# Kernel optimization log

Measured on AMD Instinct MI355X. Metric: run time of the kernel, lower is better.

## Reference

```python
import jax, jax.numpy as jnp
import numpy as np

N = 100000
E = 1600000
D_IN = 128
HID = 128
OUT = 64


def _sage_conv(x, edge_index, W_l, W_r, b, num_nodes):
    # PyG SAGEConv (aggr='mean'): out = lin_l(mean_{j in N(i)} x_j) + lin_r(x_i)
    src, dst = edge_index[0], edge_index[1]
    msgs = x[src]  # [E, d] gather from source nodes
    summed = jax.ops.segment_sum(msgs, dst, num_segments=num_nodes)  # [N, d]
    cnt = jax.ops.segment_sum(jnp.ones((msgs.shape[0],), x.dtype), dst, num_segments=num_nodes)
    agg = summed / jnp.maximum(cnt, 1.0)[:, None]  # mean; isolated nodes -> 0
    return agg @ W_l + b + x @ W_r


def setup_inputs() -> dict:
    key = jax.random.key(0)
    ks = jax.random.split(key, 8)
    x = jax.random.normal(ks[0], (N, D_IN), dtype=jnp.float32)
    edge_index = jax.random.randint(ks[1], (2, E), 0, N, dtype=jnp.int64)
    s1 = 1.0 / np.sqrt(D_IN)
    s2 = 1.0 / np.sqrt(HID)
    W_l1 = jax.random.uniform(ks[2], (D_IN, HID), jnp.float32, -s1, s1)
    W_r1 = jax.random.uniform(ks[3], (D_IN, HID), jnp.float32, -s1, s1)
    b1 = jnp.zeros((HID,), jnp.float32)
    W_l2 = jax.random.uniform(ks[4], (HID, OUT), jnp.float32, -s2, s2)
    W_r2 = jax.random.uniform(ks[5], (HID, OUT), jnp.float32, -s2, s2)
    b2 = jnp.zeros((OUT,), jnp.float32)
    return {"x": x, "edge_index": edge_index, "W_l1": W_l1, "W_r1": W_r1,
            "b1": b1, "W_l2": W_l2, "W_r2": W_r2, "b2": b2}


def reference(x, edge_index, W_l1, W_r1, b1, W_l2, W_r2, b2):
    h = _sage_conv(x, edge_index, W_l1, W_r1, b1, N)
    h = jax.nn.relu(h)
    out = _sage_conv(h, edge_index, W_l2, W_r2, b2, N)
    return out
```

## Files before the change

kernel.cpp:

```cpp
#include <hip/hip_runtime.h>
#include <hip/hip_fp16.h>

typedef __attribute__((ext_vector_type(8))) short bf16x8;
typedef __attribute__((ext_vector_type(4))) float f32x4;

__device__ __forceinline__ f32x4 mfma16(bf16x8 a, bf16x8 b, f32x4 c) {
    return __builtin_amdgcn_mfma_f32_16x16x32_bf16(a, b, c, 0, 0, 0);
}

__device__ __forceinline__ unsigned short bf16_rte(float f) {
    unsigned int u = __float_as_uint(f);
    unsigned int r = (u + 0x7FFFu + ((u >> 16) & 1u)) >> 16;
    return (unsigned short)r;
}
__device__ __forceinline__ float bf16_f(unsigned short h) {
    return __uint_as_float(((unsigned int)h) << 16);
}

__device__ __forceinline__ void split8h(bf16x8 raw, bf16x8& hi, bf16x8& lo) {
#pragma unroll
    for (int j = 0; j < 8; ++j) {
        float f = __half2float(__ushort_as_half((unsigned short)raw[j]));
        unsigned short h = bf16_rte(f);
        hi[j] = (short)h;
        lo[j] = (short)bf16_rte(f - bf16_f(h));
    }
}

__global__ void k_wconv(const float* __restrict__ W, unsigned short* __restrict__ hi,
                        unsigned short* __restrict__ lo, int K, int F) {
    int e = blockIdx.x * 256 + threadIdx.x;
    if (e >= K * F) return;
    int col = e / K, k = e - col * K;
    float v = W[(size_t)k * F + col];
    unsigned short h = bf16_rte(v);
    hi[e] = h;
    lo[e] = bf16_rte(v - bf16_f(h));
}

__global__ __launch_bounds__(256) void k_xconv(const float* __restrict__ x,
                                               unsigned short* __restrict__ x16,
                                               int total8) {
    int i = blockIdx.x * 256 + threadIdx.x;
    if (i >= total8) return;
    const float4* xp = (const float4*)x + (size_t)i * 2;
    float4 a = xp[0], b = xp[1];
    bf16x8 o;
    o[0] = (short)__half_as_ushort(__float2half_rn(a.x));
    o[1] = (short)__half_as_ushort(__float2half_rn(a.y));
    o[2] = (short)__half_as_ushort(__float2half_rn(a.z));
    o[3] = (short)__half_as_ushort(__float2half_rn(a.w));
    o[4] = (short)__half_as_ushort(__float2half_rn(b.x));
    o[5] = (short)__half_as_ushort(__float2half_rn(b.y));
    o[6] = (short)__half_as_ushort(__float2half_rn(b.z));
    o[7] = (short)__half_as_ushort(__float2half_rn(b.w));
    *(bf16x8*)&x16[(size_t)i * 8] = o;
}


#define MAXNB 1024

__global__ __launch_bounds__(256) void k_bcount(
    const int* __restrict__ dst, int* __restrict__ bcnt, int E, int chunk, int nb) {
    __shared__ int h[MAXNB];
    int t = threadIdx.x;
    for (int i = t; i < nb; i += 256) h[i] = 0;
    __syncthreads();
    int base = blockIdx.x * chunk;
    int end = min(base + chunk, E);
    for (int i = base + t; i < end; i += 256) atomicAdd(&h[dst[i] >> 7], 1);
    __syncthreads();
    for (int i = t; i < nb; i += 256)
        if (h[i]) atomicAdd(&bcnt[i], h[i]);
}

__global__ void k_bscan(const int* __restrict__ bcnt, int* __restrict__ boff,
                        int* __restrict__ bcur, int nb) {
    __shared__ int sh[1024];
    int t = threadIdx.x;
    int v = (t < nb) ? bcnt[t] : 0;
    sh[t] = v;
    __syncthreads();
    for (int off = 1; off < 1024; off <<= 1) {
        int u = (t >= off) ? sh[t - off] : 0;
        __syncthreads();
        sh[t] += u;
        __syncthreads();
    }
    if (t < nb) {
        int ex = sh[t] - v;
        boff[t] = ex;
        bcur[t] = ex;
    }
}

__global__ __launch_bounds__(256) void k_bscatter(
    const int* __restrict__ src, const int* __restrict__ dst,
    int* __restrict__ bcur, int2* __restrict__ pairs, int E, int chunk, int nb) {
    __shared__ int h[MAXNB];
    __shared__ int curs[MAXNB];
    int t = threadIdx.x;
    for (int i = t; i < nb; i += 256) h[i] = 0;
    __syncthreads();
    int base = blockIdx.x * chunk;
    int end = min(base + chunk, E);
    for (int i = base + t; i < end; i += 256) atomicAdd(&h[dst[i] >> 7], 1);
    __syncthreads();
    for (int i = t; i < nb; i += 256)
        curs[i] = h[i] ? atomicAdd(&bcur[i], h[i]) : 0;
    __syncthreads();
    for (int i = base + t; i < end; i += 256) {
        int d = dst[i];
        int p = atomicAdd(&curs[d >> 7], 1);
        pairs[p] = make_int2(d, src[i]);
    }
}

__global__ __launch_bounds__(256) void k_build(
    const int2* __restrict__ pairs, const int* __restrict__ boff,
    int* __restrict__ csr, int* __restrict__ start, int* __restrict__ deg,
    int n, int nb, int E) {
    __shared__ int scnt[128];
    __shared__ int soff[128];
    __shared__ int cur[128];
    int b = blockIdx.x;
    int t = threadIdx.x;
    int base = boff[b];
    int end = (b + 1 < nb) ? boff[b + 1] : E;
    if (t < 128) scnt[t] = 0;
    __syncthreads();
    for (int i = base + t; i < end; i += 256) {
        int2 e = pairs[i];
        atomicAdd(&scnt[e.x & 127], 1);
    }
    __syncthreads();
    if (t < 128) soff[t] = scnt[t];
    __syncthreads();
    for (int off = 1; off < 128; off <<= 1) {
        int val = 0;
        if (t < 128 && t >= off) val = soff[t - off];
        __syncthreads();
        if (t < 128) soff[t] += val;
        __syncthreads();
    }
    if (t < 128) {
        int c = scnt[t];
        int ex = soff[t] - c;
        int node = b * 128 + t;
        if (node < n) {
            start[node] = base + ex;
            deg[node] = c;
        }
        cur[t] = base + ex;
    }
    __syncthreads();
    for (int i = base + t; i < end; i += 256) {
        int2 e = pairs[i];
        int p = atomicAdd(&cur[e.x & 127], 1);
        csr[p] = e.y;
    }
}


#define SR 40

template <int FOUT, bool S0F32, bool OUT_H16>
__device__ __forceinline__ void gemm_dual_body(
    const float* __restrict__ X0f, const unsigned short* __restrict__ X0h,
    const unsigned short* __restrict__ X1h,
    const unsigned short* __restrict__ W0H, const unsigned short* __restrict__ W0L,
    const unsigned short* __restrict__ W1H, const unsigned short* __restrict__ W1L,
    const float* __restrict__ bias, unsigned short* __restrict__ dstH,
    float* __restrict__ dstF, int n) {
    constexpr int CT = FOUT / 64;
    __shared__ unsigned short aHi[4][64 * SR], aLo[4][64 * SR];

    int t = threadIdx.x;
    int wv = t >> 6, l = t & 63, q = l >> 4, nl = l & 15;
    int wc = wv * (FOUT / 4);
    int node0 = blockIdx.x * 64;
    int sn = t >> 2, q4 = t & 3;
    int gn = min(node0 + sn, n - 1);

    bf16x8 s1r[4];
    {
        const unsigned short* p = X1h + (size_t)gn * 128 + q4 * 8;
#pragma unroll
        for (int c = 0; c < 4; ++c) s1r[c] = *(const bf16x8*)(p + c * 32);
    }
    bf16x8 w1h0[CT], w1l0[CT];
#pragma unroll
    for (int uu = 0; uu < CT; ++uu) {
        int base = (wc + uu * 16 + nl) * 128 + q * 8;
        w1h0[uu] = *(const bf16x8*)&W1H[base];
        w1l0[uu] = *(const bf16x8*)&W1L[base];
    }

    if (S0F32) {
        const float4* ap = (const float4*)(X0f + (size_t)gn * 128);
        float4 xa[8];
#pragma unroll
        for (int c = 0; c < 4; ++c) {
            xa[c * 2]     = ap[c * 8 + q4 * 2];
            xa[c * 2 + 1] = ap[c * 8 + q4 * 2 + 1];
        }
        int base = sn * SR + q4 * 8;
#pragma unroll
        for (int c = 0; c < 4; ++c) {
            ushort4 hi, lo;
            float4 v = xa[c * 2];
            hi.x = bf16_rte(v.x); lo.x = bf16_rte(v.x - bf16_f(hi.x));
            hi.y = bf16_rte(v.y); lo.y = bf16_rte(v.y - bf16_f(hi.y));
            hi.z = bf16_rte(v.z); lo.z = bf16_rte(v.z - bf16_f(hi.z));
            hi.w = bf16_rte(v.w); lo.w = bf16_rte(v.w - bf16_f(hi.w));
            *(ushort4*)&aHi[c][base] = hi;
            *(ushort4*)&aLo[c][base] = lo;
            v = xa[c * 2 + 1];
            hi.x = bf16_rte(v.x); lo.x = bf16_rte(v.x - bf16_f(hi.x));
            hi.y = bf16_rte(v.y); lo.y = bf16_rte(v.y - bf16_f(hi.y));
            hi.z = bf16_rte(v.z); lo.z = bf16_rte(v.z - bf16_f(hi.z));
            hi.w = bf16_rte(v.w); lo.w = bf16_rte(v.w - bf16_f(hi.w));
            *(ushort4*)&aHi[c][base + 4] = hi;
            *(ushort4*)&aLo[c][base + 4] = lo;
        }
    } else {
        const unsigned short* p = X0h + (size_t)gn * 128 + q4 * 8;
        bf16x8 r[4];
#pragma unroll
        for (int c = 0; c < 4; ++c) r[c] = *(const bf16x8*)(p + c * 32);
        int base = sn * SR + q4 * 8;
#pragma unroll
        for (int c = 0; c < 4; ++c) {
            bf16x8 hi, lo;
            split8h(r[c], hi, lo);
            *(bf16x8*)&aHi[c][base] = hi;
            *(bf16x8*)&aLo[c][base] = lo;
        }
    }

    f32x4 acc[4][CT];
#pragma unroll
    for (int a = 0; a < 4; ++a)
#pragma unroll
        for (int b = 0; b < CT; ++b) acc[a][b] = (f32x4){0.f, 0.f, 0.f, 0.f};

    bf16x8 wh[2][CT], wl[2][CT];
#pragma unroll
    for (int uu = 0; uu < CT; ++uu) {
        int base = (wc + uu * 16 + nl) * 128 + q * 8;
        wh[0][uu] = *(const bf16x8*)&W0H[base];
        wl[0][uu] = *(const bf16x8*)&W0L[base];
    }
    __syncthreads();

#pragma unroll
    for (int c = 0; c < 4; ++c) {
        if (c < 3) {
#pragma unroll
            for (int uu = 0; uu < CT; ++uu) {
                int base = (wc + uu * 16 + nl) * 128 + (c + 1) * 32 + q * 8;
                wh[(c + 1) & 1][uu] = *(const bf16x8*)&W0H[base];
                wl[(c + 1) & 1][uu] = *(const bf16x8*)&W0L[base];
            }
        }
        bf16x8 ah[4], al[4];
#pragma unroll
        for (int tt = 0; tt < 4; ++tt) {
            int off = (tt * 16 + nl) * SR + q * 8;
            ah[tt] = *(const bf16x8*)&aHi[c][off];
            al[tt] = *(const bf16x8*)&aLo[c][off];
        }
        int cb = c & 1;
#pragma unroll
        for (int tt = 0; tt < 4; ++tt)
#pragma unroll
            for (int uu = 0; uu < CT; ++uu) {
                f32x4 a = acc[tt][uu];
                a = mfma16(al[tt], wh[cb][uu], a);
                a = mfma16(ah[tt], wl[cb][uu], a);
                a = mfma16(ah[tt], wh[cb][uu], a);
                acc[tt][uu] = a;
            }
    }
    __syncthreads();

    {
        int base = sn * SR + q4 * 8;
#pragma unroll
        for (int c = 0; c < 4; ++c) {
            bf16x8 hi, lo;
            split8h(s1r[c], hi, lo);
            *(bf16x8*)&aHi[c][base] = hi;
            *(bf16x8*)&aLo[c][base] = lo;
        }
    }
#pragma unroll
    for (int uu = 0; uu < CT; ++uu) { wh[0][uu] = w1h0[uu]; wl[0][uu] = w1l0[uu]; }
    __syncthreads();

#pragma unroll
    for (int c = 0; c < 4; ++c) {
        if (c < 3) {
#pragma unroll
            for (int uu = 0; uu < CT; ++uu) {
                int base = (wc + uu * 16 + nl) * 128 + (c + 1) * 32 + q * 8;
                wh[(c + 1) & 1][uu] = *(const bf16x8*)&W1H[base];
                wl[(c + 1) & 1][uu] = *(const bf16x8*)&W1L[base];
            }
        }
        bf16x8 ah[4], al[4];
#pragma unroll
        for (int tt = 0; tt < 4; ++tt) {
            int off = (tt * 16 + nl) * SR + q * 8;
            ah[tt] = *(const bf16x8*)&aHi[c][off];
            al[tt] = *(const bf16x8*)&aLo[c][off];
        }
        int cb = c & 1;
#pragma unroll
        for (int tt = 0; tt < 4; ++tt)
#pragma unroll
            for (int uu = 0; uu < CT; ++uu) {
                f32x4 a = acc[tt][uu];
                a = mfma16(al[tt], wh[cb][uu], a);
                a = mfma16(ah[tt], wl[cb][uu], a);
                a = mfma16(ah[tt], wh[cb][uu], a);
                acc[tt][uu] = a;
            }
    }
    __syncthreads();

    if (OUT_H16) {
        unsigned short* tb = &aHi[0][0];
#pragma unroll
        for (int uu = 0; uu < CT; ++uu) {
            int col = wc + uu * 16 + nl;
            float bv = bias[col];
#pragma unroll
            for (int tt = 0; tt < 4; ++tt)
#pragma unroll
                for (int r = 0; r < 4; ++r) {
                    float vv = fmaxf(acc[tt][uu][r] + bv, 0.f);
                    tb[(tt * 16 + q * 4 + r) * 136 + col] =
                        __half_as_ushort(__float2half_rn(vv));
                }
        }
        __syncthreads();
        int node = node0 + sn;
        if (node < n) {
            const unsigned short* sp = tb + sn * 136 + q4 * 32;
            unsigned short* dp = dstH + (size_t)node * 128 + q4 * 32;
#pragma unroll
            for (int i = 0; i < 4; ++i) *(bf16x8*)(dp + i * 8) = *(const bf16x8*)(sp + i * 8);
        }
    } else {
        float* tb = (float*)&aHi[0][0];
#pragma unroll
        for (int uu = 0; uu < CT; ++uu) {
            int col = wc + uu * 16 + nl;
            float bv = bias[col];
#pragma unroll
            for (int tt = 0; tt < 4; ++tt)
#pragma unroll
                for (int r = 0; r < 4; ++r)
                    tb[(tt * 16 + q * 4 + r) * 68 + col] = acc[tt][uu][r] + bv;
        }
        __syncthreads();
        int node = node0 + sn;
        if (node < n) {
            const float* sp = tb + sn * 68 + q4 * 16;
            float* dp = dstF + (size_t)node * 64 + q4 * 16;
#pragma unroll
            for (int i = 0; i < 4; ++i) *(float4*)(dp + i * 4) = *(const float4*)(sp + i * 4);
        }
    }
}

__global__ __launch_bounds__(256, 2) void gemm1f(
    const float* __restrict__ X, const unsigned short* __restrict__ XM,
    const unsigned short* WrH, const unsigned short* WrL,
    const unsigned short* WlH, const unsigned short* WlL,
    const float* __restrict__ bias, unsigned short* __restrict__ h16, int n) {
    gemm_dual_body<128, true, true>(X, nullptr, XM, WrH, WrL, WlH, WlL, bias, h16, nullptr, n);
}

__global__ __launch_bounds__(256, 2) void gemm2f(
    const unsigned short* __restrict__ H, const unsigned short* __restrict__ HM,
    const unsigned short* WrH, const unsigned short* WrL,
    const unsigned short* WlH, const unsigned short* WlL,
    const float* __restrict__ bias, float* __restrict__ out, int n) {
    gemm_dual_body<64, false, false>(nullptr, H, HM, WrH, WrL, WlH, WlL, bias, nullptr, out, n);
}

__global__ void aggF(const unsigned short* __restrict__ tab, const int* __restrict__ csr,
                     const int* __restrict__ start, const int* __restrict__ deg,
                     unsigned short* __restrict__ outm, int n) {
    int gid = blockIdx.x * blockDim.x + threadIdx.x;
    int wave = gid >> 6, lane = gid & 63;
    int half = lane >> 5, fl = lane & 31;
    int node = wave * 2 + half;
    if (node >= n) return;
    int s = start[node], d = deg[node];
    const float2* u2 = (const float2*)tab;
    float4 A = {0.f, 0.f, 0.f, 0.f}, B = {0.f, 0.f, 0.f, 0.f};
    int j = 0;
    for (; j + 4 <= d; j += 4) {
        int i0 = csr[s + j], i1 = csr[s + j + 1], i2 = csr[s + j + 2], i3 = csr[s + j + 3];
        float2 r0 = u2[(size_t)i0 * 32 + fl];
        float2 r1 = u2[(size_t)i1 * 32 + fl];
        float2 r2 = u2[(size_t)i2 * 32 + fl];
        float2 r3 = u2[(size_t)i3 * 32 + fl];
        float2 a0 = __half22float2(*(const __half2*)&r0.x), b0 = __half22float2(*(const __half2*)&r0.y);
        float2 a1 = __half22float2(*(const __half2*)&r1.x), b1 = __half22float2(*(const __half2*)&r1.y);
        float2 a2 = __half22float2(*(const __half2*)&r2.x), b2 = __half22float2(*(const __half2*)&r2.y);
        float2 a3 = __half22float2(*(const __half2*)&r3.x), b3 = __half22float2(*(const __half2*)&r3.y);
        A.x += a0.x + a1.x; A.y += a0.y + a1.y;
        A.z += b0.x + b1.x; A.w += b0.y + b1.y;
        B.x += a2.x + a3.x; B.y += a2.y + a3.y;
        B.z += b2.x + b3.x; B.w += b2.y + b3.y;
    }
    for (; j < d; ++j) {
        float2 r0 = u2[(size_t)csr[s + j] * 32 + fl];
        float2 a0 = __half22float2(*(const __half2*)&r0.x), b0 = __half22float2(*(const __half2*)&r0.y);
        A.x += a0.x; A.y += a0.y; A.z += b0.x; A.w += b0.y;
    }
    float inv = 1.0f / (float)max(d, 1);
    float mx = (A.x + B.x) * inv, my = (A.y + B.y) * inv;
    float mz = (A.z + B.z) * inv, mw = (A.w + B.w) * inv;
    __half2 h01 = __floats2half2_rn(mx, my);
    __half2 h23 = __floats2half2_rn(mz, mw);
    uint2 w;
    w.x = *(unsigned int*)&h01;
    w.y = *(unsigned int*)&h23;
    *(uint2*)&outm[(size_t)node * 128 + fl * 4] = w;
}


extern "C" void kernel_launch(void* const* d_in, const int* in_sizes, int n_in,
                              void* d_out, int out_size, void* d_ws, size_t ws_size,
                              hipStream_t stream) {
    const float* x   = (const float*)d_in[0];
    const int*   ei  = (const int*)d_in[1];
    const float* Wl1 = (const float*)d_in[2];
    const float* Wr1 = (const float*)d_in[3];
    const float* b1  = (const float*)d_in[4];
    const float* Wl2 = (const float*)d_in[5];
    const float* Wr2 = (const float*)d_in[6];
    const float* b2  = (const float*)d_in[7];
    float* out = (float*)d_out;

    int Nn = in_sizes[0] / 128;
    int E  = in_sizes[1] / 2;
    const int* src = ei;
    const int* dst = ei + E;
    int nb = (Nn + 127) / 128;

    char* ws = (char*)d_ws;
    auto alloc = [&](size_t bytes) -> char* {
        char* pp = ws;
        ws += (bytes + 255) / 256 * 256;
        return pp;
    };
    int* bcnt   = (int*)alloc((size_t)nb * 4);
    int* boff   = (int*)alloc((size_t)nb * 4);
    int* bcur   = (int*)alloc((size_t)nb * 4);
    int* start  = (int*)alloc((size_t)Nn * 4);
    int* deg    = (int*)alloc((size_t)Nn * 4);
    int* csr    = (int*)alloc((size_t)E * 4);
    unsigned short* x16  = (unsigned short*)alloc((size_t)Nn * 128 * 2);
    unsigned short* xm16 = (unsigned short*)alloc((size_t)Nn * 128 * 2);
    unsigned short* h16  = (unsigned short*)alloc((size_t)Nn * 128 * 2);
    unsigned short* hm16 = (unsigned short*)alloc((size_t)Nn * 128 * 2);
    unsigned short* w1ah = (unsigned short*)alloc(128 * 128 * 2);
    unsigned short* w1al = (unsigned short*)alloc(128 * 128 * 2);
    unsigned short* w1bh = (unsigned short*)alloc(128 * 128 * 2);
    unsigned short* w1bl = (unsigned short*)alloc(128 * 128 * 2);
    unsigned short* w2ah = (unsigned short*)alloc(64 * 128 * 2);
    unsigned short* w2al = (unsigned short*)alloc(64 * 128 * 2);
    unsigned short* w2bh = (unsigned short*)alloc(64 * 128 * 2);
    unsigned short* w2bl = (unsigned short*)alloc(64 * 128 * 2);
    int2* pairs = (int2*)hm16;

    hipMemsetAsync(bcnt, 0, (size_t)nb * 4, stream);

    k_wconv<<<64, 256, 0, stream>>>(Wl1, w1ah, w1al, 128, 128);
    k_wconv<<<64, 256, 0, stream>>>(Wr1, w1bh, w1bl, 128, 128);
    k_wconv<<<32, 256, 0, stream>>>(Wl2, w2ah, w2al, 128, 64);
    k_wconv<<<32, 256, 0, stream>>>(Wr2, w2bh, w2bl, 128, 64);
    k_xconv<<<(Nn * 16 + 255) / 256, 256, 0, stream>>>(x, x16, Nn * 16);

    int chunk = (E + 255) / 256;
    k_bcount<<<256, 256, 0, stream>>>(dst, bcnt, E, chunk, nb);
    k_bscan<<<1, 1024, 0, stream>>>(bcnt, boff, bcur, nb);
    k_bscatter<<<256, 256, 0, stream>>>(src, dst, bcur, pairs, E, chunk, nb);
    k_build<<<nb, 256, 0, stream>>>(pairs, boff, csr, start, deg, Nn, nb, E);

    int gb = (Nn + 63) / 64;
    aggF<<<(Nn + 7) / 8, 256, 0, stream>>>(x16, csr, start, deg, xm16, Nn);
    gemm1f<<<gb, 256, 0, stream>>>(x, xm16, w1bh, w1bl, w1ah, w1al, b1, h16, Nn);
    aggF<<<(Nn + 7) / 8, 256, 0, stream>>>(h16, csr, start, deg, hm16, Nn);
    gemm2f<<<gb, 256, 0, stream>>>(h16, hm16, w2bh, w2bl, w2ah, w2al, b2, out, Nn);
}
```

Baseline: 377.4 us.

## Merge weight conversions into one launch, feed fp16 x to gemm1, prefetch CSR indices

Four weight-conversion launches are merged into a single kernel that dispatches on block index. gemm1 now reads the fp16 copy of x instead of the fp32 input, which halves that read and reuses the split path already used by gemm2. The cost is an fp16 rounding of x before the self term, which may affect accuracy. The aggregation loop also software-prefetches the next four neighbour indices so index loads overlap the feature gathers.

```diff
diff --git a/kernel.cpp b/kernel.cpp
--- a/kernel.cpp
+++ b/kernel.cpp
@@ -27,11 +27,23 @@
     }
 }
 
-__global__ void k_wconv(const float* __restrict__ W, unsigned short* __restrict__ hi,
-                        unsigned short* __restrict__ lo, int K, int F) {
-    int e = blockIdx.x * 256 + threadIdx.x;
-    if (e >= K * F) return;
-    int col = e / K, k = e - col * K;
+__global__ __launch_bounds__(256) void k_wconv_all(
+    const float* __restrict__ Wl1, const float* __restrict__ Wr1,
+    const float* __restrict__ Wl2, const float* __restrict__ Wr2,
+    unsigned short* __restrict__ w1ah, unsigned short* __restrict__ w1al,
+    unsigned short* __restrict__ w1bh, unsigned short* __restrict__ w1bl,
+    unsigned short* __restrict__ w2ah, unsigned short* __restrict__ w2al,
+    unsigned short* __restrict__ w2bh, unsigned short* __restrict__ w2bl) {
+    int b = blockIdx.x;
+    const float* W;
+    unsigned short *hi, *lo;
+    int F, e;
+    if (b < 64)       { W = Wl1; hi = w1ah; lo = w1al; F = 128; e = b * 256 + threadIdx.x; }
+    else if (b < 128) { W = Wr1; hi = w1bh; lo = w1bl; F = 128; e = (b - 64) * 256 + threadIdx.x; }
+    else if (b < 160) { W = Wl2; hi = w2ah; lo = w2al; F = 64;  e = (b - 128) * 256 + threadIdx.x; }
+    else              { W = Wr2; hi = w2bh; lo = w2bl; F = 64;  e = (b - 160) * 256 + threadIdx.x; }
+    if (e >= 128 * F) return;
+    int col = e >> 7, k = e & 127;
     float v = W[(size_t)k * F + col];
     unsigned short h = bf16_rte(v);
     hi[e] = h;
@@ -164,10 +176,9 @@
 
 #define SR 40
 
-template <int FOUT, bool S0F32, bool OUT_H16>
+template <int FOUT, bool OUT_H16>
 __device__ __forceinline__ void gemm_dual_body(
-    const float* __restrict__ X0f, const unsigned short* __restrict__ X0h,
-    const unsigned short* __restrict__ X1h,
+    const unsigned short* __restrict__ X0h, const unsigned short* __restrict__ X1h,
     const unsigned short* __restrict__ W0H, const unsigned short* __restrict__ W0L,
     const unsigned short* __restrict__ W1H, const unsigned short* __restrict__ W1L,
     const float* __restrict__ bias, unsigned short* __restrict__ dstH,
@@ -196,34 +207,7 @@
         w1l0[uu] = *(const bf16x8*)&W1L[base];
     }
 
-    if (S0F32) {
-        const float4* ap = (const float4*)(X0f + (size_t)gn * 128);
-        float4 xa[8];
-#pragma unroll
-        for (int c = 0; c < 4; ++c) {
-            xa[c * 2]     = ap[c * 8 + q4 * 2];
-            xa[c * 2 + 1] = ap[c * 8 + q4 * 2 + 1];
-        }
-        int base = sn * SR + q4 * 8;
-#pragma unroll
-        for (int c = 0; c < 4; ++c) {
-            ushort4 hi, lo;
-            float4 v = xa[c * 2];
-            hi.x = bf16_rte(v.x); lo.x = bf16_rte(v.x - bf16_f(hi.x));
-            hi.y = bf16_rte(v.y); lo.y = bf16_rte(v.y - bf16_f(hi.y));
-            hi.z = bf16_rte(v.z); lo.z = bf16_rte(v.z - bf16_f(hi.z));
-            hi.w = bf16_rte(v.w); lo.w = bf16_rte(v.w - bf16_f(hi.w));
-            *(ushort4*)&aHi[c][base] = hi;
-            *(ushort4*)&aLo[c][base] = lo;
-            v = xa[c * 2 + 1];
-            hi.x = bf16_rte(v.x); lo.x = bf16_rte(v.x - bf16_f(hi.x));
-            hi.y = bf16_rte(v.y); lo.y = bf16_rte(v.y - bf16_f(hi.y));
-            hi.z = bf16_rte(v.z); lo.z = bf16_rte(v.z - bf16_f(hi.z));
-            hi.w = bf16_rte(v.w); lo.w = bf16_rte(v.w - bf16_f(hi.w));
-            *(ushort4*)&aHi[c][base + 4] = hi;
-            *(ushort4*)&aLo[c][base + 4] = lo;
-        }
-    } else {
+    {
         const unsigned short* p = X0h + (size_t)gn * 128 + q4 * 8;
         bf16x8 r[4];
 #pragma unroll
@@ -376,11 +360,11 @@
 }
 
 __global__ __launch_bounds__(256, 2) void gemm1f(
-    const float* __restrict__ X, const unsigned short* __restrict__ XM,
+    const unsigned short* __restrict__ X, const unsigned short* __restrict__ XM,
     const unsigned short* WrH, const unsigned short* WrL,
     const unsigned short* WlH, const unsigned short* WlL,
     const float* __restrict__ bias, unsigned short* __restrict__ h16, int n) {
-    gemm_dual_body<128, true, true>(X, nullptr, XM, WrH, WrL, WlH, WlL, bias, h16, nullptr, n);
+    gemm_dual_body<128, true>(X, XM, WrH, WrL, WlH, WlL, bias, h16, nullptr, n);
 }
 
 __global__ __launch_bounds__(256, 2) void gemm2f(
@@ -388,7 +372,7 @@
     const unsigned short* WrH, const unsigned short* WrL,
     const unsigned short* WlH, const unsigned short* WlL,
     const float* __restrict__ bias, float* __restrict__ out, int n) {
-    gemm_dual_body<64, false, false>(nullptr, H, HM, WrH, WrL, WlH, WlL, bias, nullptr, out, n);
+    gemm_dual_body<64, false>(H, HM, WrH, WrL, WlH, WlL, bias, nullptr, out, n);
 }
 
 __global__ void aggF(const unsigned short* __restrict__ tab, const int* __restrict__ csr,
@@ -403,8 +387,11 @@
     const float2* u2 = (const float2*)tab;
     float4 A = {0.f, 0.f, 0.f, 0.f}, B = {0.f, 0.f, 0.f, 0.f};
     int j = 0;
-    for (; j + 4 <= d; j += 4) {
-        int i0 = csr[s + j], i1 = csr[s + j + 1], i2 = csr[s + j + 2], i3 = csr[s + j + 3];
+    int i0 = 0, i1 = 0, i2 = 0, i3 = 0;
+    if (j + 4 <= d) { i0 = csr[s]; i1 = csr[s + 1]; i2 = csr[s + 2]; i3 = csr[s + 3]; }
+    for (; j + 8 <= d; j += 4) {
+        int n0 = csr[s + j + 4], n1 = csr[s + j + 5];
+        int n2 = csr[s + j + 6], n3 = csr[s + j + 7];
         float2 r0 = u2[(size_t)i0 * 32 + fl];
         float2 r1 = u2[(size_t)i1 * 32 + fl];
         float2 r2 = u2[(size_t)i2 * 32 + fl];
@@ -417,6 +404,22 @@
         A.z += b0.x + b1.x; A.w += b0.y + b1.y;
         B.x += a2.x + a3.x; B.y += a2.y + a3.y;
         B.z += b2.x + b3.x; B.w += b2.y + b3.y;
+        i0 = n0; i1 = n1; i2 = n2; i3 = n3;
+    }
+    if (j + 4 <= d) {
+        float2 r0 = u2[(size_t)i0 * 32 + fl];
+        float2 r1 = u2[(size_t)i1 * 32 + fl];
+        float2 r2 = u2[(size_t)i2 * 32 + fl];
+        float2 r3 = u2[(size_t)i3 * 32 + fl];
+        float2 a0 = __half22float2(*(const __half2*)&r0.x), b0 = __half22float2(*(const __half2*)&r0.y);
+        float2 a1 = __half22float2(*(const __half2*)&r1.x), b1 = __half22float2(*(const __half2*)&r1.y);
+        float2 a2 = __half22float2(*(const __half2*)&r2.x), b2 = __half22float2(*(const __half2*)&r2.y);
+        float2 a3 = __half22float2(*(const __half2*)&r3.x), b3 = __half22float2(*(const __half2*)&r3.y);
+        A.x += a0.x + a1.x; A.y += a0.y + a1.y;
+        A.z += b0.x + b1.x; A.w += b0.y + b1.y;
+        B.x += a2.x + a3.x; B.y += a2.y + a3.y;
+        B.z += b2.x + b3.x; B.w += b2.y + b3.y;
+        j += 4;
     }
     for (; j < d; ++j) {
         float2 r0 = u2[(size_t)csr[s + j] * 32 + fl];
@@ -482,10 +485,9 @@
 
     hipMemsetAsync(bcnt, 0, (size_t)nb * 4, stream);
 
-    k_wconv<<<64, 256, 0, stream>>>(Wl1, w1ah, w1al, 128, 128);
-    k_wconv<<<64, 256, 0, stream>>>(Wr1, w1bh, w1bl, 128, 128);
-    k_wconv<<<32, 256, 0, stream>>>(Wl2, w2ah, w2al, 128, 64);
-    k_wconv<<<32, 256, 0, stream>>>(Wr2, w2bh, w2bl, 128, 64);
+    k_wconv_all<<<192, 256, 0, stream>>>(Wl1, Wr1, Wl2, Wr2,
+                                         w1ah, w1al, w1bh, w1bl,
+                                         w2ah, w2al, w2bh, w2bl);
     k_xconv<<<(Nn * 16 + 255) / 256, 256, 0, stream>>>(x, x16, Nn * 16);
 
     int chunk = (E + 255) / 256;
@@ -496,7 +498,7 @@
 
     int gb = (Nn + 63) / 64;
     aggF<<<(Nn + 7) / 8, 256, 0, stream>>>(x16, csr, start, deg, xm16, Nn);
-    gemm1f<<<gb, 256, 0, stream>>>(x, xm16, w1bh, w1bl, w1ah, w1al, b1, h16, Nn);
+    gemm1f<<<gb, 256, 0, stream>>>(x16, xm16, w1bh, w1bl, w1ah, w1al, b1, h16, Nn);
     aggF<<<(Nn + 7) / 8, 256, 0, stream>>>(h16, csr, start, deg, hm16, Nn);
     gemm2f<<<gb, 256, 0, stream>>>(h16, hm16, w2bh, w2bl, w2ah, w2al, b2, out, Nn);
 }
```

Result: faster. 361.0 us (-4.4%).
